# Optimization experiments

Measured on AMD Instinct MI355X. Metric: run time of the kernel, lower is better.

## Reference

```python
import jax, jax.numpy as jnp
import numpy as np

SEQ_LEN, BATCH, TAGS = 512, 1024, 32
START_IDX, END_IDX = 30, 31
NEG = -10000.0


def setup_inputs() -> dict:
    key = jax.random.key(0)
    k1, k2 = jax.random.split(key)
    feats = jax.random.normal(k1, (SEQ_LEN, BATCH, TAGS), dtype=jnp.float32)
    mask = jnp.ones((SEQ_LEN, BATCH), dtype=jnp.float32)
    # xavier-normal-ish transition, then apply START/END constraints as in reset_parameters
    transition = jax.random.normal(k2, (TAGS, TAGS), dtype=jnp.float32) * (2.0 / (TAGS + TAGS)) ** 0.5
    transition = transition.at[START_IDX, :].set(NEG)
    transition = transition.at[:, END_IDX].set(NEG)
    return {"feats": feats, "mask": mask, "transition": transition}


def reference(feats, mask, transition):
    # feats: (T, N, M), mask: (T, N), transition: (M, M)
    batch_size, tag_size = feats.shape[1], feats.shape[2]
    alpha0 = jnp.full((batch_size, tag_size), NEG, dtype=feats.dtype)
    alpha0 = alpha0.at[:, START_IDX].set(0.0)

    def step(alpha, inp):
        feat_t, mask_t = inp  # (N, M), (N,)
        # score[n, j, i] = alpha[n, i] + transition[j, i] + feat[n, j]
        score = alpha[:, None, :] + transition[None, :, :] + feat_t[:, :, None]
        new_alpha = jax.nn.logsumexp(score, axis=-1)  # (N, M)
        m = mask_t[:, None]
        alpha = new_alpha * m + alpha * (1.0 - m)
        return alpha, None

    alpha, _ = jax.lax.scan(step, alpha0, (feats, mask))
    alpha = alpha + transition[END_IDX][None, :]
    return jax.nn.logsumexp(alpha, axis=-1)  # (N,)
```

## Files before the change

### kernel.cpp

```cpp
#include <hip/hip_runtime.h>


constexpr int SEQ = 512, BATCH = 1024, TAGS = 32;
constexpr int NC = 8, L = SEQ / NC;
constexpr int RROW = 16;

#define LOG2E 1.4426950408889634f
#define LN2   0.6931471805599453f

typedef __attribute__((ext_vector_type(8))) short short8;
typedef __attribute__((ext_vector_type(4))) float float4v;
typedef __attribute__((ext_vector_type(4))) unsigned uint4v;
union Frag8 { unsigned u[4]; short8 v; };

__device__ __forceinline__ unsigned pk_rn(float x, float y) {
  return __builtin_amdgcn_perm(__float_as_uint(y) + 0x8000u,
                               __float_as_uint(x) + 0x8000u, 0x07060302u);
}
__device__ __forceinline__ unsigned pk_tr(float x, float y) {
  return __builtin_amdgcn_perm(__float_as_uint(y), __float_as_uint(x), 0x07060302u);
}

extern "C" __global__ void __launch_bounds__(512, 6) crf_fused(
    const float* __restrict__ feats, const float* __restrict__ mask,
    const float* __restrict__ trans, float* __restrict__ out) {
  __shared__ unsigned gst[NC][66 * RROW];
  __shared__ float c2s[NC];
  __shared__ __align__(16) float ws[TAGS];
  __shared__ float c2x;

  const int wid = __builtin_amdgcn_readfirstlane((int)(threadIdx.x >> 6));
  const int lane = threadIdx.x & 63;
  const int b = blockIdx.x;
  const int s = lane & 15, q = lane >> 4;
  unsigned* Wp = &gst[wid][0];

  unsigned long long mb;
  {
    const float* fro = feats + ((size_t)(wid * L + lane) * BATCH + b) * TAGS;
    float4v fv[8];
#pragma unroll
    for (int i = 0; i < 8; ++i) fv[i] = *(const float4v*)(fro + 4 * i);
    const float mv = mask[(size_t)(wid * L + lane) * BATCH + b];
    mb = __ballot(mv != 0.0f);
    unsigned* rp = Wp + lane * RROW;
#pragma unroll
    for (int g = 0; g < 4; ++g) {
      uint4v t;
#pragma unroll
      for (int k2 = 0; k2 < 4; ++k2) {
        const int j = 4 * g + k2;
        const float lo = __builtin_amdgcn_exp2f(fv[j >> 2][j & 3] * LOG2E);
        const float hi = __builtin_amdgcn_exp2f(fv[4 + (j >> 2)][j & 3] * LOG2E);
        t[k2] = pk_rn(lo, hi);
      }
      *(uint4v*)(rp + 4 * g) = t;
    }
  }

  int sig[8];
#pragma unroll
  for (int i = 0; i < 8; ++i) sig[i] = (i < 4) ? (4 * q + i) : (16 + 4 * q + (i - 4));
  Frag8 e0, e1;
#pragma unroll
  for (int p = 0; p < 4; ++p) {
    e0.u[p] = pk_rn(__builtin_amdgcn_exp2f(trans[s * TAGS + sig[2 * p]] * LOG2E),
                    __builtin_amdgcn_exp2f(trans[s * TAGS + sig[2 * p + 1]] * LOG2E));
    e1.u[p] = pk_rn(__builtin_amdgcn_exp2f(trans[(16 + s) * TAGS + sig[2 * p]] * LOG2E),
                    __builtin_amdgcn_exp2f(trans[(16 + s) * TAGS + sig[2 * p + 1]] * LOG2E));
  }

  float4v P00 = {0, 0, 0, 0}, P01 = {0, 0, 0, 0}, P10 = {0, 0, 0, 0}, P11 = {0, 0, 0, 0};
#pragma unroll
  for (int p = 0; p < 4; ++p) {
    float one = (4 * q + p == s) ? 1.f : 0.f;
    P00[p] = one; P11[p] = one;
  }
  Frag8 B0, B1;
  float c2 = 0.f;
  const float4v zerov = {0.f, 0.f, 0.f, 0.f};

#define PACK_B()                                                        \
  { B0.u[0] = pk_tr(P00[0], P00[1]); B0.u[1] = pk_tr(P00[2], P00[3]);   \
    B0.u[2] = pk_tr(P10[0], P10[1]); B0.u[3] = pk_tr(P10[2], P10[3]);   \
    B1.u[0] = pk_tr(P01[0], P01[1]); B1.u[1] = pk_tr(P01[2], P01[3]);   \
    B1.u[2] = pk_tr(P11[0], P11[1]); B1.u[3] = pk_tr(P11[2], P11[3]); }
  PACK_B()

#define RDU(t) (*(const uint4v*)(Wp + (t) * RROW + 4 * q))

  uint4v Ua = RDU(0), Ub = RDU(1);

#pragma unroll 8
  for (int r = 0; r < L; ++r) {
    const uint4v U = (r & 1) ? Ub : Ua;
    if (r & 1) Ub = RDU(r + 2); else Ua = RDU(r + 2);

    if ((mb >> r) & 1ull) {
      float4v F0, F1;
#pragma unroll
      for (int i = 0; i < 4; ++i) {
        F0[i] = __uint_as_float(U[i] << 16);
        F1[i] = __uint_as_float(U[i] & 0xffff0000u);
      }
      float4v D00 = __builtin_amdgcn_mfma_f32_16x16x32_bf16(e0.v, B0.v, zerov, 0, 0, 0);
      float4v D01 = __builtin_amdgcn_mfma_f32_16x16x32_bf16(e0.v, B1.v, zerov, 0, 0, 0);
      float4v D10 = __builtin_amdgcn_mfma_f32_16x16x32_bf16(e1.v, B0.v, zerov, 0, 0, 0);
      float4v D11 = __builtin_amdgcn_mfma_f32_16x16x32_bf16(e1.v, B1.v, zerov, 0, 0, 0);
      P00 = D00 * F0; P01 = D01 * F0;
      P10 = D10 * F1; P11 = D11 * F1;
      PACK_B()
    }

    if ((r & 7) == 7) {
      float4v m4 = __builtin_elementwise_max(__builtin_elementwise_max(P00, P01),
                                             __builtin_elementwise_max(P10, P11));
      float mx = fmaxf(fmaxf(m4[0], m4[1]), fmaxf(m4[2], m4[3]));
      mx = fmaxf(mx, __shfl_xor(mx, 1, 64));
      mx = fmaxf(mx, __shfl_xor(mx, 2, 64));
      mx = fmaxf(mx, __shfl_xor(mx, 4, 64));
      mx = fmaxf(mx, __shfl_xor(mx, 8, 64));
      mx = fmaxf(mx, __shfl_xor(mx, 16, 64));
      mx = fmaxf(mx, __shfl_xor(mx, 32, 64));
      int ex = (int)((__float_as_uint(mx) >> 23) & 0xFFu) - 127;
      float scl = __uint_as_float((unsigned)(127 - ex) << 23);
      P00 *= scl; P01 *= scl; P10 *= scl; P11 *= scl;
      c2 += (float)ex;
      PACK_B()
    }
  }

  if (lane == 0) c2s[wid] = c2;
  if (threadIdx.x == 0) c2x = 0.f;
  __syncthreads();

  for (int k = NC - 1; k >= 0; --k) {
    if (wid == k) {
      float4v w0, w1;
      if (k == NC - 1) {
#pragma unroll
        for (int p = 0; p < 4; ++p) {
          w0[p] = __builtin_amdgcn_exp2f(trans[31 * TAGS + 4 * q + p] * LOG2E);
          w1[p] = __builtin_amdgcn_exp2f(trans[31 * TAGS + 16 + 4 * q + p] * LOG2E);
        }
      } else {
        w0 = *(const float4v*)(ws + 4 * q);
        w1 = *(const float4v*)(ws + 16 + 4 * q);
      }
      float ps = 0.f, pt = 0.f;
#pragma unroll
      for (int p = 0; p < 4; ++p) {
        ps += w0[p] * P00[p] + w1[p] * P10[p];
        pt += w0[p] * P01[p] + w1[p] * P11[p];
      }
      ps += __shfl_xor(ps, 16, 64); ps += __shfl_xor(ps, 32, 64);
      pt += __shfl_xor(pt, 16, 64); pt += __shfl_xor(pt, 32, 64);
      if (k > 0) {
        float mx = fmaxf(ps, pt);
        mx = fmaxf(mx, __shfl_xor(mx, 1, 64));
        mx = fmaxf(mx, __shfl_xor(mx, 2, 64));
        mx = fmaxf(mx, __shfl_xor(mx, 4, 64));
        mx = fmaxf(mx, __shfl_xor(mx, 8, 64));
        int ex = (int)((__float_as_uint(mx) >> 23) & 0xFFu) - 127;
        float scl = __uint_as_float((unsigned)(127 - ex) << 23);
        ps *= scl; pt *= scl;
        if (lane == 0) c2x += (float)ex;
        if (lane < 16) { ws[lane] = ps; ws[16 + lane] = pt; }
      } else if (lane == 14) {
        float c2t = ((c2s[0] + c2s[1]) + (c2s[2] + c2s[3])) +
                    ((c2s[4] + c2s[5]) + (c2s[6] + c2s[7])) + c2x;
        out[b] = LN2 * (c2t + __builtin_amdgcn_logf(pt));
      }
    }
    __syncthreads();
  }
}

extern "C" void kernel_launch(void* const* d_in, const int* in_sizes, int n_in,
                              void* d_out, int out_size, void* d_ws, size_t ws_size,
                              hipStream_t stream) {
  const float* feats = (const float*)d_in[0];
  const float* mask  = (const float*)d_in[1];
  const float* trans = (const float*)d_in[2];
  float* out = (float*)d_out;
  hipLaunchKernelGGL(crf_fused, dim3(BATCH), dim3(512), 0, stream,
                     feats, mask, trans, out);
}
```

Before: 131.2 us.

## Replace chunked transfer-matrix scan with bidirectional 16-batch vector scans and LDS prefetch ring

```diff
diff --git a/kernel.cpp b/kernel.cpp
--- a/kernel.cpp
+++ b/kernel.cpp
@@ -2,15 +2,17 @@
 
 
 constexpr int SEQ = 512, BATCH = 1024, TAGS = 32;
-constexpr int NC = 8, L = SEQ / NC;
-constexpr int RROW = 16;
+constexpr int HALF = SEQ / 2;
+constexpr int DPF = 14;
+constexpr int RING = 16;
+constexpr int SLOTF = 512;
+constexpr int SLOT = SLOTF + 64;
 
 #define LOG2E 1.4426950408889634f
 #define LN2   0.6931471805599453f
 
 typedef __attribute__((ext_vector_type(8))) short short8;
 typedef __attribute__((ext_vector_type(4))) float float4v;
-typedef __attribute__((ext_vector_type(4))) unsigned uint4v;
 union Frag8 { unsigned u[4]; short8 v; };
 
 __device__ __forceinline__ unsigned pk_rn(float x, float y) {
@@ -21,159 +23,185 @@
   return __builtin_amdgcn_perm(__float_as_uint(y), __float_as_uint(x), 0x07060302u);
 }
 
-extern "C" __global__ void __launch_bounds__(512, 6) crf_fused(
+__device__ __forceinline__ void gld16(const float* g, unsigned* l) {
+  __builtin_amdgcn_global_load_lds((const __attribute__((address_space(1))) void*)g,
+                                   (__attribute__((address_space(3))) void*)l, 16, 0, 0);
+}
+__device__ __forceinline__ void gld4(const float* g, unsigned* l) {
+  __builtin_amdgcn_global_load_lds((const __attribute__((address_space(1))) void*)g,
+                                   (__attribute__((address_space(3))) void*)l, 4, 0, 0);
+}
+
+template <bool FWD>
+__device__ __forceinline__ void run_chain(
+    const float* __restrict__ feats, const float* __restrict__ maskp,
+    const float* __restrict__ trans, float* __restrict__ out,
+    unsigned* __restrict__ ring, float* __restrict__ vbuf,
+    float* __restrict__ c2buf, int b0, int lane) {
+  const int s = lane & 15, q = lane >> 4;
+
+  const int bl = lane >> 3;
+  const int jg = (lane & 7) ^ (bl & 7);
+  const float* src0 = feats + (size_t)(b0 + bl) * TAGS + jg * 4;
+  const float* src1 = feats + (size_t)(b0 + 8 + bl) * TAGS + jg * 4;
+  const float* srcm = maskp + b0 + s;
+  const size_t fstep = (size_t)BATCH * TAGS;
+
+  const int off0 = s * 32 + ((q ^ (s & 7)) << 2);
+  const int off1 = s * 32 + (((q + 4) ^ (s & 7)) << 2);
+  const int offm = SLOTF + s + 16 * q;
+
+  auto ISSUE = [&](int r) {
+    const int rc = (r < HALF) ? r : (HALF - 1);
+    const int gt = FWD ? rc : (SEQ - 1 - rc);
+    unsigned* sl = ring + (rc & (RING - 1)) * SLOT;
+    gld16(src0 + (size_t)gt * fstep, sl);
+    gld16(src1 + (size_t)gt * fstep, sl + 256);
+    gld4(srcm + (size_t)gt * BATCH, sl + SLOTF);
+  };
+
+#pragma unroll
+  for (int d = 0; d < DPF; ++d) ISSUE(d);
+
+  int sig[8];
+#pragma unroll
+  for (int i = 0; i < 8; ++i) sig[i] = (i < 4) ? (4 * q + i) : (16 + 4 * q + (i - 4));
+  Frag8 e0, e1;
+#pragma unroll
+  for (int p = 0; p < 4; ++p) {
+    if (FWD) {
+      e0.u[p] = pk_rn(__builtin_amdgcn_exp2f(trans[s * TAGS + sig[2 * p]] * LOG2E),
+                      __builtin_amdgcn_exp2f(trans[s * TAGS + sig[2 * p + 1]] * LOG2E));
+      e1.u[p] = pk_rn(__builtin_amdgcn_exp2f(trans[(16 + s) * TAGS + sig[2 * p]] * LOG2E),
+                      __builtin_amdgcn_exp2f(trans[(16 + s) * TAGS + sig[2 * p + 1]] * LOG2E));
+    } else {
+      e0.u[p] = pk_rn(__builtin_amdgcn_exp2f(trans[sig[2 * p] * TAGS + s] * LOG2E),
+                      __builtin_amdgcn_exp2f(trans[sig[2 * p + 1] * TAGS + s] * LOG2E));
+      e1.u[p] = pk_rn(__builtin_amdgcn_exp2f(trans[sig[2 * p] * TAGS + 16 + s] * LOG2E),
+                      __builtin_amdgcn_exp2f(trans[sig[2 * p + 1] * TAGS + 16 + s] * LOG2E));
+    }
+  }
+
+  float a[8];
+#pragma unroll
+  for (int i = 0; i < 8; ++i) {
+    if (FWD) a[i] = (q == 3 && i == 6) ? 1.0f : 0.0f;
+    else a[i] = __builtin_amdgcn_exp2f(
+        trans[31 * TAGS + ((i < 4) ? (4 * q + i) : (16 + 4 * q + (i - 4)))] * LOG2E);
+  }
+  Frag8 Bf;
+  Bf.u[0] = pk_tr(a[0], a[1]); Bf.u[1] = pk_tr(a[2], a[3]);
+  Bf.u[2] = pk_tr(a[4], a[5]); Bf.u[3] = pk_tr(a[6], a[7]);
+  float c2 = 0.f;
+  const float4v zerov = {0.f, 0.f, 0.f, 0.f};
+
+  asm volatile("s_waitcnt vmcnt(39)" ::: "memory");
+  float4v Fc0, Fc1;
+  float mc;
+  {
+    const unsigned* sl = ring;
+    const float4v r0 = *(const float4v*)(const void*)(sl + off0);
+    const float4v r1 = *(const float4v*)(const void*)(sl + off1);
+    const unsigned mw = sl[offm];
+#pragma unroll
+    for (int i = 0; i < 4; ++i) {
+      Fc0[i] = __builtin_amdgcn_exp2f(r0[i] * LOG2E);
+      Fc1[i] = __builtin_amdgcn_exp2f(r1[i] * LOG2E);
+    }
+    mc = __uint_as_float(mw);
+  }
+
+#pragma unroll 2
+  for (int r = 0; r < HALF; ++r) {
+    ISSUE(r + DPF);
+    asm volatile("s_waitcnt vmcnt(39)" ::: "memory");
+    const unsigned* sl = ring + ((r + 1) & (RING - 1)) * SLOT;
+    const float4v r0 = *(const float4v*)(const void*)(sl + off0);
+    const float4v r1 = *(const float4v*)(const void*)(sl + off1);
+    const unsigned mw = sl[offm];
+
+    const bool mv = (mc != 0.0f);
+    if (FWD) {
+      const float4v D0 = __builtin_amdgcn_mfma_f32_16x16x32_bf16(e0.v, Bf.v, zerov, 0, 0, 0);
+      const float4v D1 = __builtin_amdgcn_mfma_f32_16x16x32_bf16(e1.v, Bf.v, zerov, 0, 0, 0);
+#pragma unroll
+      for (int i = 0; i < 4; ++i) {
+        a[i]     = mv ? D0[i] * Fc0[i] : a[i];
+        a[4 + i] = mv ? D1[i] * Fc1[i] : a[4 + i];
+      }
+    } else {
+      float tb[8];
+#pragma unroll
+      for (int i = 0; i < 4; ++i) { tb[i] = a[i] * Fc0[i]; tb[4 + i] = a[4 + i] * Fc1[i]; }
+      Frag8 Bp;
+      Bp.u[0] = pk_tr(tb[0], tb[1]); Bp.u[1] = pk_tr(tb[2], tb[3]);
+      Bp.u[2] = pk_tr(tb[4], tb[5]); Bp.u[3] = pk_tr(tb[6], tb[7]);
+      const float4v D0 = __builtin_amdgcn_mfma_f32_16x16x32_bf16(e0.v, Bp.v, zerov, 0, 0, 0);
+      const float4v D1 = __builtin_amdgcn_mfma_f32_16x16x32_bf16(e1.v, Bp.v, zerov, 0, 0, 0);
+#pragma unroll
+      for (int i = 0; i < 4; ++i) {
+        a[i]     = mv ? D0[i] : a[i];
+        a[4 + i] = mv ? D1[i] : a[4 + i];
+      }
+    }
+
+    if ((r & 7) == 7) {
+      float mx = fmaxf(fmaxf(fmaxf(a[0], a[1]), fmaxf(a[2], a[3])),
+                       fmaxf(fmaxf(a[4], a[5]), fmaxf(a[6], a[7])));
+      mx = fmaxf(mx, __shfl_xor(mx, 16, 64));
+      mx = fmaxf(mx, __shfl_xor(mx, 32, 64));
+      const int ex = (int)((__float_as_uint(mx) >> 23) & 0xFFu) - 127;
+      const float scl = __uint_as_float((unsigned)(127 - ex) << 23);
+#pragma unroll
+      for (int i = 0; i < 8; ++i) a[i] *= scl;
+      c2 += (float)ex;
+    }
+
+    if (FWD) {
+      Bf.u[0] = pk_tr(a[0], a[1]); Bf.u[1] = pk_tr(a[2], a[3]);
+      Bf.u[2] = pk_tr(a[4], a[5]); Bf.u[3] = pk_tr(a[6], a[7]);
+    }
+
+#pragma unroll
+    for (int i = 0; i < 4; ++i) {
+      Fc0[i] = __builtin_amdgcn_exp2f(r0[i] * LOG2E);
+      Fc1[i] = __builtin_amdgcn_exp2f(r1[i] * LOG2E);
+    }
+    mc = __uint_as_float(mw);
+  }
+
+  if (!FWD) {
+    float4v lo = {a[0], a[1], a[2], a[3]}, hi = {a[4], a[5], a[6], a[7]};
+    *(float4v*)(vbuf + lane * 8) = lo;
+    *(float4v*)(vbuf + lane * 8 + 4) = hi;
+    if (lane < 16) c2buf[lane] = c2;
+  }
+  __syncthreads();
+  if (FWD) {
+    const float4v v0 = *(const float4v*)(vbuf + lane * 8);
+    const float4v v1 = *(const float4v*)(vbuf + lane * 8 + 4);
+    float dot = a[0] * v0[0] + a[1] * v0[1] + a[2] * v0[2] + a[3] * v0[3] +
+                a[4] * v1[0] + a[5] * v1[1] + a[6] * v1[2] + a[7] * v1[3];
+    dot += __shfl_xor(dot, 16, 64);
+    dot += __shfl_xor(dot, 32, 64);
+    if (lane < 16)
+      out[b0 + lane] = LN2 * (c2 + c2buf[lane] + __builtin_amdgcn_logf(dot));
+  }
+}
+
+extern "C" __global__ void __launch_bounds__(128) crf_scan(
     const float* __restrict__ feats, const float* __restrict__ mask,
     const float* __restrict__ trans, float* __restrict__ out) {
-  __shared__ unsigned gst[NC][66 * RROW];
-  __shared__ float c2s[NC];
-  __shared__ __align__(16) float ws[TAGS];
-  __shared__ float c2x;
-
-  const int wid = __builtin_amdgcn_readfirstlane((int)(threadIdx.x >> 6));
+  __shared__ unsigned ring2[2][RING * SLOT];
+  __shared__ float vbuf[512];
+  __shared__ float c2buf[16];
+  const int wid = threadIdx.x >> 6;
   const int lane = threadIdx.x & 63;
-  const int b = blockIdx.x;
-  const int s = lane & 15, q = lane >> 4;
-  unsigned* Wp = &gst[wid][0];
-
-  unsigned long long mb;
-  {
-    const float* fro = feats + ((size_t)(wid * L + lane) * BATCH + b) * TAGS;
-    float4v fv[8];
-#pragma unroll
-    for (int i = 0; i < 8; ++i) fv[i] = *(const float4v*)(fro + 4 * i);
-    const float mv = mask[(size_t)(wid * L + lane) * BATCH + b];
-    mb = __ballot(mv != 0.0f);
-    unsigned* rp = Wp + lane * RROW;
-#pragma unroll
-    for (int g = 0; g < 4; ++g) {
-      uint4v t;
-#pragma unroll
-      for (int k2 = 0; k2 < 4; ++k2) {
-        const int j = 4 * g + k2;
-        const float lo = __builtin_amdgcn_exp2f(fv[j >> 2][j & 3] * LOG2E);
-        const float hi = __builtin_amdgcn_exp2f(fv[4 + (j >> 2)][j & 3] * LOG2E);
-        t[k2] = pk_rn(lo, hi);
-      }
-      *(uint4v*)(rp + 4 * g) = t;
-    }
-  }
-
-  int sig[8];
-#pragma unroll
-  for (int i = 0; i < 8; ++i) sig[i] = (i < 4) ? (4 * q + i) : (16 + 4 * q + (i - 4));
-  Frag8 e0, e1;
-#pragma unroll
-  for (int p = 0; p < 4; ++p) {
-    e0.u[p] = pk_rn(__builtin_amdgcn_exp2f(trans[s * TAGS + sig[2 * p]] * LOG2E),
-                    __builtin_amdgcn_exp2f(trans[s * TAGS + sig[2 * p + 1]] * LOG2E));
-    e1.u[p] = pk_rn(__builtin_amdgcn_exp2f(trans[(16 + s) * TAGS + sig[2 * p]] * LOG2E),
-                    __builtin_amdgcn_exp2f(trans[(16 + s) * TAGS + sig[2 * p + 1]] * LOG2E));
-  }
-
-  float4v P00 = {0, 0, 0, 0}, P01 = {0, 0, 0, 0}, P10 = {0, 0, 0, 0}, P11 = {0, 0, 0, 0};
-#pragma unroll
-  for (int p = 0; p < 4; ++p) {
-    float one = (4 * q + p == s) ? 1.f : 0.f;
-    P00[p] = one; P11[p] = one;
-  }
-  Frag8 B0, B1;
-  float c2 = 0.f;
-  const float4v zerov = {0.f, 0.f, 0.f, 0.f};
-
-#define PACK_B()                                                        \
-  { B0.u[0] = pk_tr(P00[0], P00[1]); B0.u[1] = pk_tr(P00[2], P00[3]);   \
-    B0.u[2] = pk_tr(P10[0], P10[1]); B0.u[3] = pk_tr(P10[2], P10[3]);   \
-    B1.u[0] = pk_tr(P01[0], P01[1]); B1.u[1] = pk_tr(P01[2], P01[3]);   \
-    B1.u[2] = pk_tr(P11[0], P11[1]); B1.u[3] = pk_tr(P11[2], P11[3]); }
-  PACK_B()
-
-#define RDU(t) (*(const uint4v*)(Wp + (t) * RROW + 4 * q))
-
-  uint4v Ua = RDU(0), Ub = RDU(1);
-
-#pragma unroll 8
-  for (int r = 0; r < L; ++r) {
-    const uint4v U = (r & 1) ? Ub : Ua;
-    if (r & 1) Ub = RDU(r + 2); else Ua = RDU(r + 2);
-
-    if ((mb >> r) & 1ull) {
-      float4v F0, F1;
-#pragma unroll
-      for (int i = 0; i < 4; ++i) {
-        F0[i] = __uint_as_float(U[i] << 16);
-        F1[i] = __uint_as_float(U[i] & 0xffff0000u);
-      }
-      float4v D00 = __builtin_amdgcn_mfma_f32_16x16x32_bf16(e0.v, B0.v, zerov, 0, 0, 0);
-      float4v D01 = __builtin_amdgcn_mfma_f32_16x16x32_bf16(e0.v, B1.v, zerov, 0, 0, 0);
-      float4v D10 = __builtin_amdgcn_mfma_f32_16x16x32_bf16(e1.v, B0.v, zerov, 0, 0, 0);
-      float4v D11 = __builtin_amdgcn_mfma_f32_16x16x32_bf16(e1.v, B1.v, zerov, 0, 0, 0);
-      P00 = D00 * F0; P01 = D01 * F0;
-      P10 = D10 * F1; P11 = D11 * F1;
-      PACK_B()
-    }
-
-    if ((r & 7) == 7) {
-      float4v m4 = __builtin_elementwise_max(__builtin_elementwise_max(P00, P01),
-                                             __builtin_elementwise_max(P10, P11));
-      float mx = fmaxf(fmaxf(m4[0], m4[1]), fmaxf(m4[2], m4[3]));
-      mx = fmaxf(mx, __shfl_xor(mx, 1, 64));
-      mx = fmaxf(mx, __shfl_xor(mx, 2, 64));
-      mx = fmaxf(mx, __shfl_xor(mx, 4, 64));
-      mx = fmaxf(mx, __shfl_xor(mx, 8, 64));
-      mx = fmaxf(mx, __shfl_xor(mx, 16, 64));
-      mx = fmaxf(mx, __shfl_xor(mx, 32, 64));
-      int ex = (int)((__float_as_uint(mx) >> 23) & 0xFFu) - 127;
-      float scl = __uint_as_float((unsigned)(127 - ex) << 23);
-      P00 *= scl; P01 *= scl; P10 *= scl; P11 *= scl;
-      c2 += (float)ex;
-      PACK_B()
-    }
-  }
-
-  if (lane == 0) c2s[wid] = c2;
-  if (threadIdx.x == 0) c2x = 0.f;
-  __syncthreads();
-
-  for (int k = NC - 1; k >= 0; --k) {
-    if (wid == k) {
-      float4v w0, w1;
-      if (k == NC - 1) {
-#pragma unroll
-        for (int p = 0; p < 4; ++p) {
-          w0[p] = __builtin_amdgcn_exp2f(trans[31 * TAGS + 4 * q + p] * LOG2E);
-          w1[p] = __builtin_amdgcn_exp2f(trans[31 * TAGS + 16 + 4 * q + p] * LOG2E);
-        }
-      } else {
-        w0 = *(const float4v*)(ws + 4 * q);
-        w1 = *(const float4v*)(ws + 16 + 4 * q);
-      }
-      float ps = 0.f, pt = 0.f;
-#pragma unroll
-      for (int p = 0; p < 4; ++p) {
-        ps += w0[p] * P00[p] + w1[p] * P10[p];
-        pt += w0[p] * P01[p] + w1[p] * P11[p];
-      }
-      ps += __shfl_xor(ps, 16, 64); ps += __shfl_xor(ps, 32, 64);
-      pt += __shfl_xor(pt, 16, 64); pt += __shfl_xor(pt, 32, 64);
-      if (k > 0) {
-        float mx = fmaxf(ps, pt);
-        mx = fmaxf(mx, __shfl_xor(mx, 1, 64));
-        mx = fmaxf(mx, __shfl_xor(mx, 2, 64));
-        mx = fmaxf(mx, __shfl_xor(mx, 4, 64));
-        mx = fmaxf(mx, __shfl_xor(mx, 8, 64));
-        int ex = (int)((__float_as_uint(mx) >> 23) & 0xFFu) - 127;
-        float scl = __uint_as_float((unsigned)(127 - ex) << 23);
-        ps *= scl; pt *= scl;
-        if (lane == 0) c2x += (float)ex;
-        if (lane < 16) { ws[lane] = ps; ws[16 + lane] = pt; }
-      } else if (lane == 14) {
-        float c2t = ((c2s[0] + c2s[1]) + (c2s[2] + c2s[3])) +
-                    ((c2s[4] + c2s[5]) + (c2s[6] + c2s[7])) + c2x;
-        out[b] = LN2 * (c2t + __builtin_amdgcn_logf(pt));
-      }
-    }
-    __syncthreads();
-  }
+  const int b0 = blockIdx.x * 16;
+  if (wid == 0)
+    run_chain<true>(feats, mask, trans, out, &ring2[0][0], vbuf, c2buf, b0, lane);
+  else
+    run_chain<false>(feats, mask, trans, out, &ring2[1][0], vbuf, c2buf, b0, lane);
 }
 
 extern "C" void kernel_launch(void* const* d_in, const int* in_sizes, int n_in,
@@ -183,6 +211,6 @@
   const float* mask  = (const float*)d_in[1];
   const float* trans = (const float*)d_in[2];
   float* out = (float*)d_out;
-  hipLaunchKernelGGL(crf_fused, dim3(BATCH), dim3(512), 0, stream,
+  hipLaunchKernelGGL(crf_scan, dim3(BATCH / 16), dim3(128), 0, stream,
                      feats, mask, trans, out);
 }
```

Measured after the change: 180.4 us. 1.38x slower.
